# Optimization experiments

Hardware: AMD Instinct MI355X
Metric: run time of the kernel (lower is better)

The kernel has to match this reference:

```python
import jax, jax.numpy as jnp
import numpy as np

N, E, DIN, DH, DOUT = 100000, 600000, 128, 128, 64


def _glorot(k, shape):
    lim = float(np.sqrt(6.0 / (shape[0] + shape[1])))
    return jax.random.uniform(k, shape, jnp.float32, -lim, lim)


def setup_inputs() -> dict:
    key = jax.random.key(0)
    ks = jax.random.split(key, 12)
    return {
        "x": jax.random.normal(ks[0], (N, DIN), jnp.float32),
        "src": jax.random.randint(ks[1], (E,), 0, N),
        "dst": jax.random.randint(ks[2], (E,), 0, N),
        # layer 0: NGNN_SAGEConv = SAGEConv(in,hid) + fc(hid,hid) + fc2(hid,hid)
        "w_self0": _glorot(ks[3], (DIN, DH)), "b_self0": jnp.zeros((DH,), jnp.float32),
        "w_neigh0": _glorot(ks[4], (DIN, DH)),
        "fc_w": _glorot(ks[5], (DH, DH)), "fc_b": jnp.zeros((DH,), jnp.float32),
        "fc2_w": _glorot(ks[6], (DH, DH)), "fc2_b": jnp.zeros((DH,), jnp.float32),
        # layer 1: SAGEConv(hid,hid)
        "w_self1": _glorot(ks[7], (DH, DH)), "b_self1": jnp.zeros((DH,), jnp.float32),
        "w_neigh1": _glorot(ks[8], (DH, DH)),
        # layer 2: SAGEConv(hid,out)
        "w_self2": _glorot(ks[9], (DH, DOUT)), "b_self2": jnp.zeros((DOUT,), jnp.float32),
        "w_neigh2": _glorot(ks[10], (DH, DOUT)),
    }


def _sage_conv(x, src, dst, w_self, b_self, w_neigh):
    # DGL SAGEConv, aggregator='mean': out = x @ W_self + b + mean_{u->v} x_u @ W_neigh
    agg = jax.ops.segment_sum(x[src], dst, num_segments=N)          # [N, d_in]
    deg = jax.ops.segment_sum(jnp.ones((src.shape[0],), x.dtype), dst, num_segments=N)
    h_neigh = agg / jnp.maximum(deg, 1.0)[:, None]                  # zero-in-degree -> 0
    return x @ w_self + b_self + h_neigh @ w_neigh


def reference(x, src, dst,
              w_self0, b_self0, w_neigh0, fc_w, fc_b, fc2_w, fc2_b,
              w_self1, b_self1, w_neigh1,
              w_self2, b_self2, w_neigh2):
    # layer 0: NGNN_SAGEConv with num_nonl_layers=2, then outer ReLU (dropout: eval = identity)
    h = _sage_conv(x, src, dst, w_self0, b_self0, w_neigh0)
    h = jax.nn.relu(h)
    h = h @ fc_w + fc_b
    h = jax.nn.relu(h)
    h = h @ fc2_w + fc2_b
    h = jax.nn.relu(h)
    # layer 1: SAGEConv + ReLU
    h = _sage_conv(h, src, dst, w_self1, b_self1, w_neigh1)
    h = jax.nn.relu(h)
    # layer 2 (output): SAGEConv, no activation
    return _sage_conv(h, src, dst, w_self2, b_self2, w_neigh2)
```

## Files before the change

### kernel.cpp

```cpp
#include <hip/hip_runtime.h>

#define N_NODES 100000
#define N_EDGES 600000
#define K_DIM   128
#define NPART   ((N_NODES + 255) / 256)
#define EBLK    ((N_EDGES + 255) / 256)
#define CASTB   (N_NODES * K_DIM / 8 / 256)
#define GBLK    ((N_NODES + 127) / 128)
#define VROWS   (GBLK * 128)

typedef unsigned short ushort_t;
typedef short v8s __attribute__((ext_vector_type(8)));
typedef float v4f __attribute__((ext_vector_type(4)));

__device__ __forceinline__ ushort_t f2b(float f) {
  unsigned u = __builtin_bit_cast(unsigned, f);
  unsigned r = u + 0x7FFFu + ((u >> 16) & 1u);
  return (ushort_t)(r >> 16);
}
__device__ __forceinline__ float b2f(ushort_t h) {
  return __builtin_bit_cast(float, (unsigned)h << 16);
}
__device__ __forceinline__ float blo(unsigned u) {
  return __builtin_bit_cast(float, u << 16);
}
__device__ __forceinline__ float bhi(unsigned u) {
  return __builtin_bit_cast(float, u & 0xFFFF0000u);
}
__device__ __forceinline__ unsigned pk2(float lo, float hi) {
  return (unsigned)f2b(lo) | ((unsigned)f2b(hi) << 16);
}


__global__ void deg_cast_kernel(const int* __restrict__ dst, int* __restrict__ deg,
                                const float* __restrict__ X, ushort_t* __restrict__ Xb) {
  if (blockIdx.x < EBLK) {
    int e = blockIdx.x * 256 + threadIdx.x;
    if (e < N_EDGES) atomicAdd(&deg[dst[e]], 1);
  } else {
    int i = ((blockIdx.x - EBLK) * 256 + threadIdx.x) * 8;
    if (i >= N_NODES * K_DIM) return;
    float4 v0 = *(const float4*)(X + i);
    float4 v1 = *(const float4*)(X + i + 4);
    ushort4 h0, h1;
    h0.x = f2b(v0.x); h0.y = f2b(v0.y); h0.z = f2b(v0.z); h0.w = f2b(v0.w);
    h1.x = f2b(v1.x); h1.y = f2b(v1.y); h1.z = f2b(v1.z); h1.w = f2b(v1.w);
    *(ushort4*)(Xb + i)     = h0;
    *(ushort4*)(Xb + i + 4) = h1;
  }
}

__global__ void scan1_swz_kernel(
    const int* __restrict__ deg, int* __restrict__ excl, int* __restrict__ partials,
    const float* __restrict__ w0, const float* __restrict__ w1,
    const float* __restrict__ w2, const float* __restrict__ w3,
    const float* __restrict__ w4, const float* __restrict__ w5,
    const float* __restrict__ w6, const float* __restrict__ w7,
    ushort_t* __restrict__ s0, ushort_t* __restrict__ s1,
    ushort_t* __restrict__ s2, ushort_t* __restrict__ s3,
    ushort_t* __restrict__ s4, ushort_t* __restrict__ s5,
    ushort_t* __restrict__ s6, ushort_t* __restrict__ s7) {
  __shared__ int s[256];
  if (blockIdx.x < NPART) {
    int t = threadIdx.x, i = blockIdx.x * 256 + t;
    int v = (i < N_NODES) ? deg[i] : 0;
    s[t] = v;
    __syncthreads();
    for (int off = 1; off < 256; off <<= 1) {
      int x = (t >= off) ? s[t - off] : 0;
      __syncthreads();
      s[t] += x;
      __syncthreads();
    }
    if (i < N_NODES) excl[i] = s[t] - v;
    if (t == 255) partials[blockIdx.x] = s[t];
  } else {
    const int blk = blockIdx.x - NPART;
    const int z = blk >> 6;
    const float* W;
    ushort_t* S;
    int dout = 128;
    switch (z) {
      case 0: W = w0; S = s0; break;
      case 1: W = w1; S = s1; break;
      case 2: W = w2; S = s2; break;
      case 3: W = w3; S = s3; break;
      case 4: W = w4; S = s4; break;
      case 5: W = w5; S = s5; break;
      case 6: W = w6; S = s6; dout = 64; break;
      default: W = w7; S = s7; dout = 64; break;
    }
    int t = (blk & 63) * 256 + threadIdx.x;
    if (t >= K_DIM * dout) return;
    int k = t / dout, n = t % dout;
    S[(k >> 3) * (dout * 8) + n * 8 + (k & 7)] = f2b(W[t]);
  }
}

__global__ void scan2_kernel(int* __restrict__ partials) {
  __shared__ int s[512];
  int t = threadIdx.x;
  int v = (t < NPART) ? partials[t] : 0;
  s[t] = v;
  __syncthreads();
  for (int off = 1; off < 512; off <<= 1) {
    int x = (t >= off) ? s[t - off] : 0;
    __syncthreads();
    s[t] += x;
    __syncthreads();
  }
  if (t < NPART) partials[t] = s[t] - v;
}

__global__ void scan3_kernel(const int* __restrict__ excl, const int* __restrict__ partials,
                             const int* __restrict__ deg, int* __restrict__ row_ptr,
                             int* __restrict__ cursor, float* __restrict__ inv_deg) {
  int i = blockIdx.x * blockDim.x + threadIdx.x;
  if (i < N_NODES) {
    int rp = excl[i] + partials[i >> 8];
    row_ptr[i] = rp;
    cursor[i] = rp;
    inv_deg[i] = 1.0f / (float)(deg[i] > 1 ? deg[i] : 1);
  } else if (i == N_NODES) {
    row_ptr[N_NODES] = N_EDGES;
  }
}

__global__ void fill_kernel(const int* __restrict__ src, const int* __restrict__ dst,
                            int* __restrict__ cursor, int* __restrict__ ssrc) {
  int e = blockIdx.x * blockDim.x + threadIdx.x;
  if (e < N_EDGES) {
    int p = atomicAdd(&cursor[dst[e]], 1);
    ssrc[p] = src[e];
  }
}


template <int DOUT, bool RELU, bool BF16_OUT>
__global__ __launch_bounds__(512, 8) void sage_layer_kernel(
    const ushort_t* __restrict__ H,
    ushort_t* __restrict__ AGG,
    const ushort_t* __restrict__ Wself_sw, const ushort_t* __restrict__ Wneigh_sw,
    const float* __restrict__ bias,
    const int* __restrict__ row_ptr, const int* __restrict__ ssrc,
    const float* __restrict__ inv_deg,
    ushort_t* __restrict__ Obf, float* __restrict__ Ofp) {
  constexpr int NT  = DOUT / 16;
  constexpr int SWN = K_DIM * DOUT;
  constexpr int NW  = SWN / 4096;
  __shared__ __align__(16) ushort_t buf[16384];

  const int tid   = threadIdx.x;
  const int wv    = tid >> 6;
  const int lane  = tid & 63;
  const int lm    = lane & 15;
  const int q     = lane >> 4;
  const int lrow0 = wv * 16;
  const int row0  = blockIdx.x * 128 + lrow0;

  #pragma unroll
  for (int j = 0; j < NW; ++j)
    *(uint4*)&buf[tid * 8 + j * 4096] = *(const uint4*)&Wself_sw[tid * 8 + j * 4096];
  uint4 wreg[NW];
  #pragma unroll
  for (int j = 0; j < NW; ++j)
    wreg[j] = *(const uint4*)&Wneigh_sw[tid * 8 + j * 4096];
  __syncthreads();

  {
    const int c0 = lm * 8;
    for (int rr = 0; rr < 4; ++rr) {
      const int lr = q * 4 + rr;
      const int gv = row0 + lr;
      const int vv = gv < N_NODES ? gv : N_NODES - 1;
      float a[8];
      #pragma unroll
      for (int i = 0; i < 8; ++i) a[i] = 0.f;
      const int beg = row_ptr[vv], end = row_ptr[vv + 1];
      int e = beg;
      for (; e + 4 <= end; e += 4) {
        const int s0 = ssrc[e];
        const int s1 = ssrc[e + 1];
        const int s2 = ssrc[e + 2];
        const int s3 = ssrc[e + 3];
        const uint4 p0 = *(const uint4*)(H + (size_t)s0 * K_DIM + c0);
        const uint4 p1 = *(const uint4*)(H + (size_t)s1 * K_DIM + c0);
        const uint4 p2 = *(const uint4*)(H + (size_t)s2 * K_DIM + c0);
        const uint4 p3 = *(const uint4*)(H + (size_t)s3 * K_DIM + c0);
        a[0] += (blo(p0.x) + blo(p1.x)) + (blo(p2.x) + blo(p3.x));
        a[1] += (bhi(p0.x) + bhi(p1.x)) + (bhi(p2.x) + bhi(p3.x));
        a[2] += (blo(p0.y) + blo(p1.y)) + (blo(p2.y) + blo(p3.y));
        a[3] += (bhi(p0.y) + bhi(p1.y)) + (bhi(p2.y) + bhi(p3.y));
        a[4] += (blo(p0.z) + blo(p1.z)) + (blo(p2.z) + blo(p3.z));
        a[5] += (bhi(p0.z) + bhi(p1.z)) + (bhi(p2.z) + bhi(p3.z));
        a[6] += (blo(p0.w) + blo(p1.w)) + (blo(p2.w) + blo(p3.w));
        a[7] += (bhi(p0.w) + bhi(p1.w)) + (bhi(p2.w) + bhi(p3.w));
      }
      if (e + 2 <= end) {
        const int s0 = ssrc[e];
        const int s1 = ssrc[e + 1];
        const uint4 p0 = *(const uint4*)(H + (size_t)s0 * K_DIM + c0);
        const uint4 p1 = *(const uint4*)(H + (size_t)s1 * K_DIM + c0);
        a[0] += blo(p0.x) + blo(p1.x);
        a[1] += bhi(p0.x) + bhi(p1.x);
        a[2] += blo(p0.y) + blo(p1.y);
        a[3] += bhi(p0.y) + bhi(p1.y);
        a[4] += blo(p0.z) + blo(p1.z);
        a[5] += bhi(p0.z) + bhi(p1.z);
        a[6] += blo(p0.w) + blo(p1.w);
        a[7] += bhi(p0.w) + bhi(p1.w);
        e += 2;
      }
      if (e < end) {
        const int s0 = ssrc[e];
        const uint4 p0 = *(const uint4*)(H + (size_t)s0 * K_DIM + c0);
        a[0] += blo(p0.x);
        a[1] += bhi(p0.x);
        a[2] += blo(p0.y);
        a[3] += bhi(p0.y);
        a[4] += blo(p0.z);
        a[5] += bhi(p0.z);
        a[6] += blo(p0.w);
        a[7] += bhi(p0.w);
      }
      const float sc = inv_deg[vv];
      uint4 ov;
      ov.x = pk2(a[0] * sc, a[1] * sc);
      ov.y = pk2(a[2] * sc, a[3] * sc);
      ov.z = pk2(a[4] * sc, a[5] * sc);
      ov.w = pk2(a[6] * sc, a[7] * sc);
      *(uint4*)&AGG[(size_t)gv * K_DIM + c0] = ov;
    }
  }

  int ra = row0 + lm;  ra = ra < N_NODES ? ra : N_NODES - 1;
  const size_t off0 = (size_t)ra * K_DIM;

  v4f acc[NT];
  #pragma unroll
  for (int n = 0; n < NT; ++n) acc[n] = (v4f){0.f, 0.f, 0.f, 0.f};

  for (int ks = 0; ks < K_DIM / 32; ++ks) {
    const int ko = ks * 32 + q * 8;
    const v8s a0 = *(const v8s*)(H + off0 + ko);
    #pragma unroll
    for (int nt = 0; nt < NT; ++nt) {
      const v8s b = *(const v8s*)&buf[((ks * 4 + q) * DOUT + nt * 16 + lm) * 8];
      acc[nt] = __builtin_amdgcn_mfma_f32_16x16x32_bf16(a0, b, acc[nt], 0, 0, 0);
    }
  }
  __syncthreads();

  #pragma unroll
  for (int j = 0; j < NW; ++j)
    *(uint4*)&buf[tid * 8 + j * 4096] = wreg[j];
  __syncthreads();

  const size_t offA = (size_t)(row0 + lm) * K_DIM;
  for (int ks = 0; ks < K_DIM / 32; ++ks) {
    const int ko = ks * 32 + q * 8;
    const v8s a0 = *(const v8s*)(AGG + offA + ko);
    #pragma unroll
    for (int nt = 0; nt < NT; ++nt) {
      const v8s b = *(const v8s*)&buf[((ks * 4 + q) * DOUT + nt * 16 + lm) * 8];
      acc[nt] = __builtin_amdgcn_mfma_f32_16x16x32_bf16(a0, b, acc[nt], 0, 0, 0);
    }
  }
  __syncthreads();

  const int base = blockIdx.x * 128;
  if constexpr (BF16_OUT) {
    #pragma unroll
    for (int nt = 0; nt < NT; ++nt) {
      const int col = nt * 16 + lm;
      const float bv = bias[col];
      #pragma unroll
      for (int r = 0; r < 4; ++r) {
        float v = acc[nt][r] + bv;
        if (RELU) v = v > 0.f ? v : 0.f;
        buf[(lrow0 + q * 4 + r) * DOUT + col] = f2b(v);
      }
    }
    __syncthreads();
    #pragma unroll
    for (int i = tid * 8; i < 128 * DOUT; i += 4096) {
      const int rw = i / DOUT;
      if (base + rw < N_NODES)
        *(uint4*)&Obf[(size_t)(base + rw) * DOUT + (i % DOUT)] = *(const uint4*)&buf[i];
    }
  } else {
    float* fb = (float*)buf;
    #pragma unroll
    for (int nt = 0; nt < NT; ++nt) {
      const int col = nt * 16 + lm;
      const float bv = bias[col];
      #pragma unroll
      for (int r = 0; r < 4; ++r) {
        float v = acc[nt][r] + bv;
        if (RELU) v = v > 0.f ? v : 0.f;
        fb[(lrow0 + q * 4 + r) * DOUT + col] = v;
      }
    }
    __syncthreads();
    #pragma unroll
    for (int i = tid * 4; i < 128 * DOUT; i += 2048) {
      const int rw = i / DOUT;
      if (base + rw < N_NODES)
        *(float4*)&Ofp[(size_t)(base + rw) * DOUT + (i % DOUT)] = *(const float4*)&fb[i];
    }
  }
}


__global__ __launch_bounds__(512, 4) void fused_fc_kernel(
    const ushort_t* __restrict__ A,
    const ushort_t* __restrict__ W1sw, const ushort_t* __restrict__ W2sw,
    const float* __restrict__ b1, const float* __restrict__ b2,
    ushort_t* __restrict__ O) {
  constexpr int NT = 8;
  constexpr int HP = 136;
  __shared__ ushort_t bufW[K_DIM * 128];
  __shared__ ushort_t bufH[128 * HP];

  const int tid   = threadIdx.x;
  const int wv    = tid >> 6;
  const int lane  = tid & 63;
  const int lm    = lane & 15;
  const int q     = lane >> 4;
  const int lrow0 = wv * 16;
  const int row0  = blockIdx.x * 128 + lrow0;

  for (int i = tid * 8; i < K_DIM * 128; i += 4096)
    *(uint4*)&bufW[i] = *(const uint4*)&W1sw[i];

  uint4 wreg[4];
  #pragma unroll
  for (int j = 0; j < 4; ++j)
    wreg[j] = *(const uint4*)&W2sw[tid * 8 + j * 4096];

  __syncthreads();

  int ra = row0 + lm;  ra = ra < N_NODES ? ra : N_NODES - 1;
  const size_t off0 = (size_t)ra * K_DIM;

  v4f acc[NT];
  #pragma unroll
  for (int n = 0; n < NT; ++n) acc[n] = (v4f){0.f, 0.f, 0.f, 0.f};

  for (int ks = 0; ks < K_DIM / 32; ++ks) {
    const int ko = ks * 32 + q * 8;
    const v8s a0 = *(const v8s*)(A + off0 + ko);
    #pragma unroll
    for (int nt = 0; nt < NT; ++nt) {
      const v8s b = *(const v8s*)&bufW[((ks * 4 + q) * 128 + nt * 16 + lm) * 8];
      acc[nt] = __builtin_amdgcn_mfma_f32_16x16x32_bf16(a0, b, acc[nt], 0, 0, 0);
    }
  }
  __syncthreads();

  #pragma unroll
  for (int j = 0; j < 4; ++j)
    *(uint4*)&bufW[tid * 8 + j * 4096] = wreg[j];
  #pragma unroll
  for (int nt = 0; nt < NT; ++nt) {
    const int col = nt * 16 + lm;
    const float bv = b1[col];
    #pragma unroll
    for (int r = 0; r < 4; ++r) {
      float v = acc[nt][r] + bv;
      v = v > 0.f ? v : 0.f;
      bufH[(lrow0 + q * 4 + r) * HP + col] = f2b(v);
      acc[nt][r] = 0.f;
    }
  }
  __syncthreads();

  for (int ks = 0; ks < K_DIM / 32; ++ks) {
    const int ko = ks * 32 + q * 8;
    const v8s a0 = *(const v8s*)&bufH[(lrow0 + lm) * HP + ko];
    #pragma unroll
    for (int nt = 0; nt < NT; ++nt) {
      const v8s b = *(const v8s*)&bufW[((ks * 4 + q) * 128 + nt * 16 + lm) * 8];
      acc[nt] = __builtin_amdgcn_mfma_f32_16x16x32_bf16(a0, b, acc[nt], 0, 0, 0);
    }
  }

  #pragma unroll
  for (int nt = 0; nt < NT; ++nt) {
    const int col = nt * 16 + lm;
    const float bv = b2[col];
    #pragma unroll
    for (int r = 0; r < 4; ++r) {
      const int row = row0 + q * 4 + r;
      if (row < N_NODES) {
        float v = acc[nt][r] + bv;
        v = v > 0.f ? v : 0.f;
        O[(size_t)row * 128 + col] = f2b(v);
      }
    }
  }
}


extern "C" void kernel_launch(void* const* d_in, const int* in_sizes, int n_in,
                              void* d_out, int out_size, void* d_ws, size_t ws_size,
                              hipStream_t stream) {
  const float* x        = (const float*)d_in[0];
  const int*   src      = (const int*)d_in[1];
  const int*   dst      = (const int*)d_in[2];
  const float* w_self0  = (const float*)d_in[3];
  const float* b_self0  = (const float*)d_in[4];
  const float* w_neigh0 = (const float*)d_in[5];
  const float* fc_w     = (const float*)d_in[6];
  const float* fc_b     = (const float*)d_in[7];
  const float* fc2_w    = (const float*)d_in[8];
  const float* fc2_b    = (const float*)d_in[9];
  const float* w_self1  = (const float*)d_in[10];
  const float* b_self1  = (const float*)d_in[11];
  const float* w_neigh1 = (const float*)d_in[12];
  const float* w_self2  = (const float*)d_in[13];
  const float* b_self2  = (const float*)d_in[14];
  const float* w_neigh2 = (const float*)d_in[15];

  char* p = (char*)d_ws;
  auto carve = [&](size_t bytes) {
    void* q = (void*)p;
    p += (bytes + 511) & ~(size_t)511;
    return q;
  };
  const size_t PLANE = (size_t)N_NODES * K_DIM * sizeof(ushort_t);
  ushort_t* X    = (ushort_t*)carve(PLANE);
  ushort_t* Y    = (ushort_t*)carve(PLANE);
  ushort_t* Z    = (ushort_t*)carve(PLANE);
  ushort_t* AGGs = (ushort_t*)carve((size_t)VROWS * K_DIM * sizeof(ushort_t));
  ushort_t* ws0 = (ushort_t*)carve(K_DIM * 128 * 2);
  ushort_t* wn0 = (ushort_t*)carve(K_DIM * 128 * 2);
  ushort_t* wfc = (ushort_t*)carve(K_DIM * 128 * 2);
  ushort_t* wf2 = (ushort_t*)carve(K_DIM * 128 * 2);
  ushort_t* ws1 = (ushort_t*)carve(K_DIM * 128 * 2);
  ushort_t* wn1 = (ushort_t*)carve(K_DIM * 128 * 2);
  ushort_t* ws2 = (ushort_t*)carve(K_DIM * 64 * 2);
  ushort_t* wn2 = (ushort_t*)carve(K_DIM * 64 * 2);
  int*   ssrc    = (int*)carve((size_t)N_EDGES * 4);
  int*   row_ptr = (int*)carve((size_t)(N_NODES + 1) * 4);
  int*   cursor  = (int*)carve((size_t)N_NODES * 4);
  int*   deg     = (int*)carve((size_t)N_NODES * 4);
  int*   excl    = (int*)carve((size_t)N_NODES * 4);
  int*   parts   = (int*)carve(512 * 4);
  float* inv_deg = (float*)carve((size_t)N_NODES * 4);

  hipMemsetAsync(deg, 0, (size_t)N_NODES * 4, stream);
  deg_cast_kernel<<<EBLK + CASTB, 256, 0, stream>>>(dst, deg, x, X);
  scan1_swz_kernel<<<NPART + 512, 256, 0, stream>>>(
      deg, excl, parts,
      w_self0, w_neigh0, fc_w, fc2_w, w_self1, w_neigh1, w_self2, w_neigh2,
      ws0, wn0, wfc, wf2, ws1, wn1, ws2, wn2);
  scan2_kernel<<<1, 512, 0, stream>>>(parts);
  scan3_kernel<<<((N_NODES + 1) + 255) / 256, 256, 0, stream>>>(excl, parts, deg,
                                                                row_ptr, cursor, inv_deg);
  fill_kernel<<<EBLK, 256, 0, stream>>>(src, dst, cursor, ssrc);

  const int GB = GBLK;

  sage_layer_kernel<128, true, true><<<GB, 512, 0, stream>>>(
      X, AGGs, ws0, wn0, b_self0, row_ptr, ssrc, inv_deg, Z, nullptr);
  fused_fc_kernel<<<GB, 512, 0, stream>>>(Z, wfc, wf2, fc_b, fc2_b, Y);
  sage_layer_kernel<128, true, true><<<GB, 512, 0, stream>>>(
      Y, AGGs, ws1, wn1, b_self1, row_ptr, ssrc, inv_deg, Z, nullptr);
  sage_layer_kernel<64, false, false><<<GB, 512, 0, stream>>>(
      Z, AGGs, ws2, wn2, b_self2, row_ptr, ssrc, inv_deg, nullptr, (float*)d_out);
}
```

Baseline: 369.6 us.

## Fuse layer-0 SAGE conv with both NGNN fc layers into one kernel

Merges the first SAGE layer and the two-layer fc MLP into a single ngnn0_kernel. Each block aggregates neighbours, then runs the self, neighbour, fc and fc2 matmuls in sequence, reloading each weight matrix into one 32 KB LDS buffer while prefetching the next into registers. Intermediate activations are staged through a global scratch plane (HS) rather than LDS, so work buffers are padded to VROWS and the launch-bounds occupancy hint drops from 8 to 6. This removes one kernel launch and a separate pass over Z, but adds extra syncs and global round-trips for the intermediates.

After: 403.2 us. +9.1%, slower.

```diff
diff --git a/kernel.cpp b/kernel.cpp
--- a/kernel.cpp
+++ b/kernel.cpp
@@ -135,9 +135,78 @@
   }
 }
 
+__device__ __forceinline__ void agg_rows(
+    const ushort_t* __restrict__ H, ushort_t* __restrict__ AGG,
+    const int* __restrict__ row_ptr, const int* __restrict__ ssrc,
+    const float* __restrict__ inv_deg, int row0, int lm, int q) {
+  const int c0 = lm * 8;
+  for (int rr = 0; rr < 4; ++rr) {
+    const int lr = q * 4 + rr;
+    const int gv = row0 + lr;
+    const int vv = gv < N_NODES ? gv : N_NODES - 1;
+    float a[8];
+    #pragma unroll
+    for (int i = 0; i < 8; ++i) a[i] = 0.f;
+    const int beg = row_ptr[vv], end = row_ptr[vv + 1];
+    int e = beg;
+    for (; e + 4 <= end; e += 4) {
+      const int s0 = ssrc[e];
+      const int s1 = ssrc[e + 1];
+      const int s2 = ssrc[e + 2];
+      const int s3 = ssrc[e + 3];
+      const uint4 p0 = *(const uint4*)(H + (size_t)s0 * K_DIM + c0);
+      const uint4 p1 = *(const uint4*)(H + (size_t)s1 * K_DIM + c0);
+      const uint4 p2 = *(const uint4*)(H + (size_t)s2 * K_DIM + c0);
+      const uint4 p3 = *(const uint4*)(H + (size_t)s3 * K_DIM + c0);
+      a[0] += (blo(p0.x) + blo(p1.x)) + (blo(p2.x) + blo(p3.x));
+      a[1] += (bhi(p0.x) + bhi(p1.x)) + (bhi(p2.x) + bhi(p3.x));
+      a[2] += (blo(p0.y) + blo(p1.y)) + (blo(p2.y) + blo(p3.y));
+      a[3] += (bhi(p0.y) + bhi(p1.y)) + (bhi(p2.y) + bhi(p3.y));
+      a[4] += (blo(p0.z) + blo(p1.z)) + (blo(p2.z) + blo(p3.z));
+      a[5] += (bhi(p0.z) + bhi(p1.z)) + (bhi(p2.z) + bhi(p3.z));
+      a[6] += (blo(p0.w) + blo(p1.w)) + (blo(p2.w) + blo(p3.w));
+      a[7] += (bhi(p0.w) + bhi(p1.w)) + (bhi(p2.w) + bhi(p3.w));
+    }
+    if (e + 2 <= end) {
+      const int s0 = ssrc[e];
+      const int s1 = ssrc[e + 1];
+      const uint4 p0 = *(const uint4*)(H + (size_t)s0 * K_DIM + c0);
+      const uint4 p1 = *(const uint4*)(H + (size_t)s1 * K_DIM + c0);
+      a[0] += blo(p0.x) + blo(p1.x);
+      a[1] += bhi(p0.x) + bhi(p1.x);
+      a[2] += blo(p0.y) + blo(p1.y);
+      a[3] += bhi(p0.y) + bhi(p1.y);
+      a[4] += blo(p0.z) + blo(p1.z);
+      a[5] += bhi(p0.z) + bhi(p1.z);
+      a[6] += blo(p0.w) + blo(p1.w);
+      a[7] += bhi(p0.w) + bhi(p1.w);
+      e += 2;
+    }
+    if (e < end) {
+      const int s0 = ssrc[e];
+      const uint4 p0 = *(const uint4*)(H + (size_t)s0 * K_DIM + c0);
+      a[0] += blo(p0.x);
+      a[1] += bhi(p0.x);
+      a[2] += blo(p0.y);
+      a[3] += bhi(p0.y);
+      a[4] += blo(p0.z);
+      a[5] += bhi(p0.z);
+      a[6] += blo(p0.w);
+      a[7] += bhi(p0.w);
+    }
+    const float sc = inv_deg[vv];
+    uint4 ov;
+    ov.x = pk2(a[0] * sc, a[1] * sc);
+    ov.y = pk2(a[2] * sc, a[3] * sc);
+    ov.z = pk2(a[4] * sc, a[5] * sc);
+    ov.w = pk2(a[6] * sc, a[7] * sc);
+    *(uint4*)&AGG[(size_t)gv * K_DIM + c0] = ov;
+  }
+}
+
 
 template <int DOUT, bool RELU, bool BF16_OUT>
-__global__ __launch_bounds__(512, 8) void sage_layer_kernel(
+__global__ __launch_bounds__(512, 6) void sage_layer_kernel(
     const ushort_t* __restrict__ H,
     ushort_t* __restrict__ AGG,
     const ushort_t* __restrict__ Wself_sw, const ushort_t* __restrict__ Wneigh_sw,
@@ -167,71 +236,7 @@
     wreg[j] = *(const uint4*)&Wneigh_sw[tid * 8 + j * 4096];
   __syncthreads();
 
-  {
-    const int c0 = lm * 8;
-    for (int rr = 0; rr < 4; ++rr) {
-      const int lr = q * 4 + rr;
-      const int gv = row0 + lr;
-      const int vv = gv < N_NODES ? gv : N_NODES - 1;
-      float a[8];
-      #pragma unroll
-      for (int i = 0; i < 8; ++i) a[i] = 0.f;
-      const int beg = row_ptr[vv], end = row_ptr[vv + 1];
-      int e = beg;
-      for (; e + 4 <= end; e += 4) {
-        const int s0 = ssrc[e];
-        const int s1 = ssrc[e + 1];
-        const int s2 = ssrc[e + 2];
-        const int s3 = ssrc[e + 3];
-        const uint4 p0 = *(const uint4*)(H + (size_t)s0 * K_DIM + c0);
-        const uint4 p1 = *(const uint4*)(H + (size_t)s1 * K_DIM + c0);
-        const uint4 p2 = *(const uint4*)(H + (size_t)s2 * K_DIM + c0);
-        const uint4 p3 = *(const uint4*)(H + (size_t)s3 * K_DIM + c0);
-        a[0] += (blo(p0.x) + blo(p1.x)) + (blo(p2.x) + blo(p3.x));
-        a[1] += (bhi(p0.x) + bhi(p1.x)) + (bhi(p2.x) + bhi(p3.x));
-        a[2] += (blo(p0.y) + blo(p1.y)) + (blo(p2.y) + blo(p3.y));
-        a[3] += (bhi(p0.y) + bhi(p1.y)) + (bhi(p2.y) + bhi(p3.y));
-        a[4] += (blo(p0.z) + blo(p1.z)) + (blo(p2.z) + blo(p3.z));
-        a[5] += (bhi(p0.z) + bhi(p1.z)) + (bhi(p2.z) + bhi(p3.z));
-        a[6] += (blo(p0.w) + blo(p1.w)) + (blo(p2.w) + blo(p3.w));
-        a[7] += (bhi(p0.w) + bhi(p1.w)) + (bhi(p2.w) + bhi(p3.w));
-      }
-      if (e + 2 <= end) {
-        const int s0 = ssrc[e];
-        const int s1 = ssrc[e + 1];
-        const uint4 p0 = *(const uint4*)(H + (size_t)s0 * K_DIM + c0);
-        const uint4 p1 = *(const uint4*)(H + (size_t)s1 * K_DIM + c0);
-        a[0] += blo(p0.x) + blo(p1.x);
-        a[1] += bhi(p0.x) + bhi(p1.x);
-        a[2] += blo(p0.y) + blo(p1.y);
-        a[3] += bhi(p0.y) + bhi(p1.y);
-        a[4] += blo(p0.z) + blo(p1.z);
-        a[5] += bhi(p0.z) + bhi(p1.z);
-        a[6] += blo(p0.w) + blo(p1.w);
-        a[7] += bhi(p0.w) + bhi(p1.w);
-        e += 2;
-      }
-      if (e < end) {
-        const int s0 = ssrc[e];
-        const uint4 p0 = *(const uint4*)(H + (size_t)s0 * K_DIM + c0);
-        a[0] += blo(p0.x);
-        a[1] += bhi(p0.x);
-        a[2] += blo(p0.y);
-        a[3] += bhi(p0.y);
-        a[4] += blo(p0.z);
-        a[5] += bhi(p0.z);
-        a[6] += blo(p0.w);
-        a[7] += bhi(p0.w);
-      }
-      const float sc = inv_deg[vv];
-      uint4 ov;
-      ov.x = pk2(a[0] * sc, a[1] * sc);
-      ov.y = pk2(a[2] * sc, a[3] * sc);
-      ov.z = pk2(a[4] * sc, a[5] * sc);
-      ov.w = pk2(a[6] * sc, a[7] * sc);
-      *(uint4*)&AGG[(size_t)gv * K_DIM + c0] = ov;
-    }
-  }
+  agg_rows(H, AGG, row_ptr, ssrc, inv_deg, row0, lm, q);
 
   int ra = row0 + lm;  ra = ra < N_NODES ? ra : N_NODES - 1;
   const size_t off0 = (size_t)ra * K_DIM;
@@ -312,15 +317,19 @@
 }
 
 
-__global__ __launch_bounds__(512, 4) void fused_fc_kernel(
-    const ushort_t* __restrict__ A,
-    const ushort_t* __restrict__ W1sw, const ushort_t* __restrict__ W2sw,
-    const float* __restrict__ b1, const float* __restrict__ b2,
+__global__ __launch_bounds__(512, 6) void ngnn0_kernel(
+    const ushort_t* __restrict__ H,
+    ushort_t* __restrict__ AGG,
+    ushort_t* __restrict__ HS,
+    const ushort_t* __restrict__ Wself_sw, const ushort_t* __restrict__ Wneigh_sw,
+    const ushort_t* __restrict__ Wf1_sw,   const ushort_t* __restrict__ Wf2_sw,
+    const float* __restrict__ b0, const float* __restrict__ bf1,
+    const float* __restrict__ bf2,
+    const int* __restrict__ row_ptr, const int* __restrict__ ssrc,
+    const float* __restrict__ inv_deg,
     ushort_t* __restrict__ O) {
   constexpr int NT = 8;
-  constexpr int HP = 136;
-  __shared__ ushort_t bufW[K_DIM * 128];
-  __shared__ ushort_t bufH[128 * HP];
+  __shared__ __align__(16) ushort_t buf[16384];
 
   const int tid   = threadIdx.x;
   const int wv    = tid >> 6;
@@ -330,18 +339,20 @@
   const int lrow0 = wv * 16;
   const int row0  = blockIdx.x * 128 + lrow0;
 
-  for (int i = tid * 8; i < K_DIM * 128; i += 4096)
-    *(uint4*)&bufW[i] = *(const uint4*)&W1sw[i];
-
+  #pragma unroll
+  for (int j = 0; j < 4; ++j)
+    *(uint4*)&buf[tid * 8 + j * 4096] = *(const uint4*)&Wself_sw[tid * 8 + j * 4096];
   uint4 wreg[4];
   #pragma unroll
   for (int j = 0; j < 4; ++j)
-    wreg[j] = *(const uint4*)&W2sw[tid * 8 + j * 4096];
-
-  __syncthreads();
+    wreg[j] = *(const uint4*)&Wneigh_sw[tid * 8 + j * 4096];
+  __syncthreads();
+
+  agg_rows(H, AGG, row_ptr, ssrc, inv_deg, row0, lm, q);
 
   int ra = row0 + lm;  ra = ra < N_NODES ? ra : N_NODES - 1;
   const size_t off0 = (size_t)ra * K_DIM;
+  const size_t offV = (size_t)(row0 + lm) * K_DIM;
 
   v4f acc[NT];
   #pragma unroll
@@ -349,38 +360,57 @@
 
   for (int ks = 0; ks < K_DIM / 32; ++ks) {
     const int ko = ks * 32 + q * 8;
-    const v8s a0 = *(const v8s*)(A + off0 + ko);
-    #pragma unroll
-    for (int nt = 0; nt < NT; ++nt) {
-      const v8s b = *(const v8s*)&bufW[((ks * 4 + q) * 128 + nt * 16 + lm) * 8];
+    const v8s a0 = *(const v8s*)(H + off0 + ko);
+    #pragma unroll
+    for (int nt = 0; nt < NT; ++nt) {
+      const v8s b = *(const v8s*)&buf[((ks * 4 + q) * 128 + nt * 16 + lm) * 8];
       acc[nt] = __builtin_amdgcn_mfma_f32_16x16x32_bf16(a0, b, acc[nt], 0, 0, 0);
     }
   }
   __syncthreads();
-
-  #pragma unroll
-  for (int j = 0; j < 4; ++j)
-    *(uint4*)&bufW[tid * 8 + j * 4096] = wreg[j];
+  #pragma unroll
+  for (int j = 0; j < 4; ++j) {
+    *(uint4*)&buf[tid * 8 + j * 4096] = wreg[j];
+    wreg[j] = *(const uint4*)&Wf1_sw[tid * 8 + j * 4096];
+  }
+  __syncthreads();
+
+  for (int ks = 0; ks < K_DIM / 32; ++ks) {
+    const int ko = ks * 32 + q * 8;
+    const v8s a0 = *(const v8s*)(AGG + offV + ko);
+    #pragma unroll
+    for (int nt = 0; nt < NT; ++nt) {
+      const v8s b = *(const v8s*)&buf[((ks * 4 + q) * 128 + nt * 16 + lm) * 8];
+      acc[nt] = __builtin_amdgcn_mfma_f32_16x16x32_bf16(a0, b, acc[nt], 0, 0, 0);
+    }
+  }
+
   #pragma unroll
   for (int nt = 0; nt < NT; ++nt) {
     const int col = nt * 16 + lm;
-    const float bv = b1[col];
+    const float bv = b0[col];
     #pragma unroll
     for (int r = 0; r < 4; ++r) {
       float v = acc[nt][r] + bv;
       v = v > 0.f ? v : 0.f;
-      bufH[(lrow0 + q * 4 + r) * HP + col] = f2b(v);
+      HS[(size_t)(row0 + q * 4 + r) * K_DIM + col] = f2b(v);
       acc[nt][r] = 0.f;
     }
+  }
+  __syncthreads();
+  #pragma unroll
+  for (int j = 0; j < 4; ++j) {
+    *(uint4*)&buf[tid * 8 + j * 4096] = wreg[j];
+    wreg[j] = *(const uint4*)&Wf2_sw[tid * 8 + j * 4096];
   }
   __syncthreads();
 
   for (int ks = 0; ks < K_DIM / 32; ++ks) {
     const int ko = ks * 32 + q * 8;
-    const v8s a0 = *(const v8s*)&bufH[(lrow0 + lm) * HP + ko];
-    #pragma unroll
-    for (int nt = 0; nt < NT; ++nt) {
-      const v8s b = *(const v8s*)&bufW[((ks * 4 + q) * 128 + nt * 16 + lm) * 8];
+    const v8s a0 = *(const v8s*)(HS + offV + ko);
+    #pragma unroll
+    for (int nt = 0; nt < NT; ++nt) {
+      const v8s b = *(const v8s*)&buf[((ks * 4 + q) * 128 + nt * 16 + lm) * 8];
       acc[nt] = __builtin_amdgcn_mfma_f32_16x16x32_bf16(a0, b, acc[nt], 0, 0, 0);
     }
   }
@@ -388,16 +418,50 @@
   #pragma unroll
   for (int nt = 0; nt < NT; ++nt) {
     const int col = nt * 16 + lm;
-    const float bv = b2[col];
+    const float bv = bf1[col];
     #pragma unroll
     for (int r = 0; r < 4; ++r) {
-      const int row = row0 + q * 4 + r;
-      if (row < N_NODES) {
-        float v = acc[nt][r] + bv;
-        v = v > 0.f ? v : 0.f;
-        O[(size_t)row * 128 + col] = f2b(v);
-      }
-    }
+      float v = acc[nt][r] + bv;
+      v = v > 0.f ? v : 0.f;
+      HS[(size_t)(row0 + q * 4 + r) * K_DIM + col] = f2b(v);
+      acc[nt][r] = 0.f;
+    }
+  }
+  __syncthreads();
+  #pragma unroll
+  for (int j = 0; j < 4; ++j)
+    *(uint4*)&buf[tid * 8 + j * 4096] = wreg[j];
+  __syncthreads();
+
+  for (int ks = 0; ks < K_DIM / 32; ++ks) {
+    const int ko = ks * 32 + q * 8;
+    const v8s a0 = *(const v8s*)(HS + offV + ko);
+    #pragma unroll
+    for (int nt = 0; nt < NT; ++nt) {
+      const v8s b = *(const v8s*)&buf[((ks * 4 + q) * 128 + nt * 16 + lm) * 8];
+      acc[nt] = __builtin_amdgcn_mfma_f32_16x16x32_bf16(a0, b, acc[nt], 0, 0, 0);
+    }
+  }
+  __syncthreads();
+
+  const int base = blockIdx.x * 128;
+  #pragma unroll
+  for (int nt = 0; nt < NT; ++nt) {
+    const int col = nt * 16 + lm;
+    const float bv = bf2[col];
+    #pragma unroll
+    for (int r = 0; r < 4; ++r) {
+      float v = acc[nt][r] + bv;
+      v = v > 0.f ? v : 0.f;
+      buf[(lrow0 + q * 4 + r) * 128 + col] = f2b(v);
+    }
+  }
+  __syncthreads();
+  #pragma unroll
+  for (int i = tid * 8; i < 128 * 128; i += 4096) {
+    const int rw = i / 128;
+    if (base + rw < N_NODES)
+      *(uint4*)&O[(size_t)(base + rw) * 128 + (i % 128)] = *(const uint4*)&buf[i];
   }
 }
 
@@ -428,11 +492,11 @@
     p += (bytes + 511) & ~(size_t)511;
     return q;
   };
-  const size_t PLANE = (size_t)N_NODES * K_DIM * sizeof(ushort_t);
-  ushort_t* X    = (ushort_t*)carve(PLANE);
-  ushort_t* Y    = (ushort_t*)carve(PLANE);
-  ushort_t* Z    = (ushort_t*)carve(PLANE);
-  ushort_t* AGGs = (ushort_t*)carve((size_t)VROWS * K_DIM * sizeof(ushort_t));
+  const size_t VPLANE = (size_t)VROWS * K_DIM * sizeof(ushort_t);
+  ushort_t* X    = (ushort_t*)carve(VPLANE);
+  ushort_t* Y    = (ushort_t*)carve(VPLANE);
+  ushort_t* Z    = (ushort_t*)carve(VPLANE);
+  ushort_t* AGGs = (ushort_t*)carve(VPLANE);
   ushort_t* ws0 = (ushort_t*)carve(K_DIM * 128 * 2);
   ushort_t* wn0 = (ushort_t*)carve(K_DIM * 128 * 2);
   ushort_t* wfc = (ushort_t*)carve(K_DIM * 128 * 2);
@@ -462,9 +526,9 @@
 
   const int GB = GBLK;
 
-  sage_layer_kernel<128, true, true><<<GB, 512, 0, stream>>>(
-      X, AGGs, ws0, wn0, b_self0, row_ptr, ssrc, inv_deg, Z, nullptr);
-  fused_fc_kernel<<<GB, 512, 0, stream>>>(Z, wfc, wf2, fc_b, fc2_b, Y);
+  ngnn0_kernel<<<GB, 512, 0, stream>>>(
+      X, AGGs, Z, ws0, wn0, wfc, wf2, b_self0, fc_b, fc2_b,
+      row_ptr, ssrc, inv_deg, Y);
   sage_layer_kernel<128, true, true><<<GB, 512, 0, stream>>>(
       Y, AGGs, ws1, wn1, b_self1, row_ptr, ssrc, inv_deg, Z, nullptr);
   sage_layer_kernel<64, false, false><<<GB, 512, 0, stream>>>(
```
